# Kernel tuning notes

Hardware: AMD Instinct MI355X
Metric: run time of the kernel (lower is better)

## Reference

```python
import jax, jax.numpy as jnp
import numpy as np

B, TE, TD = 16, 400, 64
E, H = 256, 512
H2 = 2 * H  # 1024
V = 32000


def setup_inputs():
    key = jax.random.key(0)
    k = jax.random.split(key, 16)
    s = 0.05
    return {
        "encoder_inputs": jax.random.randint(k[0], (B, TE), 0, V),
        "decoder_inputs": jax.random.randint(k[1], (B, TD), 0, V),
        "ext_oov_sizes": jax.random.randint(k[2], (B,), 0, 10),
        "enc_idxes_on_ext_voc": jax.random.randint(k[3], (B, TE), 0, V),
        "h0": jnp.zeros((2, B, H), jnp.float32),
        "c0": jnp.zeros((2, B, H), jnp.float32),
        "emb": jax.random.normal(k[4], (V, E)) * 0.1,
        "Wih_f": jax.random.normal(k[5], (4 * H, E)) * s,
        "Whh_f": jax.random.normal(k[6], (4 * H, H)) * s,
        "b_f": jnp.zeros((4 * H,), jnp.float32),
        "Wih_b": jax.random.normal(k[7], (4 * H, E)) * s,
        "Whh_b": jax.random.normal(k[8], (4 * H, H)) * s,
        "b_b": jnp.zeros((4 * H,), jnp.float32),
        "Wih_d": jax.random.normal(k[9], (4 * H2, E + 2 * H2)) * s,
        "Whh_d": jax.random.normal(k[10], (4 * H2, H2)) * s,
        "b_d": jnp.zeros((4 * H2,), jnp.float32),
        "W_ea": jax.random.normal(k[11], (H2, H2)) * 0.006,
        "W_da": jax.random.normal(k[12], (H2, H2)) * 0.006,
        "W_v": jax.random.normal(k[13], (V, 3 * H2)) * s,
        "b_v": jnp.zeros((V,), jnp.float32),
    }


def lstm_cell(x, h, c, Wih, Whh, b):
    z = x @ Wih.T + h @ Whh.T + b
    i, f, g, o = jnp.split(z, 4, axis=-1)
    i, f, o = jax.nn.sigmoid(i), jax.nn.sigmoid(f), jax.nn.sigmoid(o)
    c2 = f * c + i * jnp.tanh(g)
    return o * jnp.tanh(c2), c2


def run_lstm(xs, h0, c0, Wih, Whh, b):
    # xs: [T, B, E]
    def step(carry, x):
        h, c = lstm_cell(x, carry[0], carry[1], Wih, Whh, b)
        return (h, c), h
    (h, c), hs = jax.lax.scan(step, (h0, c0), xs)
    return hs, h, c


def _forward(emb, Wih_f, Whh_f, b_f, Wih_b, Whh_b, b_b, Wih_d, Whh_d, b_d,
             W_ea, W_da, W_v, b_v, h0, c0, encoder_inputs, decoder_inputs):
    xs = emb[encoder_inputs].transpose(1, 0, 2)  # [TE, B, E]
    hs_f, hf, cf = run_lstm(xs, h0[0], c0[0], Wih_f, Whh_f, b_f)
    hs_b, hb, cb = run_lstm(xs[::-1], h0[1], c0[1], Wih_b, Whh_b, b_b)
    enc_out = jnp.concatenate([hs_f, hs_b[::-1]], axis=-1).transpose(1, 0, 2)  # [B, TE, 2H]
    h = jnp.concatenate([hf, hb], axis=-1)  # [B, 2H] (torch reshape of bi-dir last hidden)
    c = jnp.concatenate([cf, cb], axis=-1)
    dec_emb = emb[decoder_inputs].transpose(1, 0, 2)  # [TD, B, E]

    def step(carry, xs_t):
        h, c, accum, buf = carry
        i, emb_t = xs_t
        # intra-temporal encoder attention: exp scores normalized by past accumulation
        scores = jnp.einsum('bd,btd->bt', h @ W_ea, enc_out)  # [B, TE]
        exp_s = jnp.exp(scores)
        denom = jnp.where(i == 0, jnp.ones_like(accum), accum)
        ep = exp_s / denom
        attn = ep / jnp.sum(ep, axis=-1, keepdims=True)
        ctx_e = jnp.einsum('bt,btd->bd', attn, enc_out)
        # intra-decoder attention over previously produced hidden states (masked)
        dsc = jnp.einsum('bd,tbd->bt', h @ W_da, buf)  # [B, TD]
        dsc = jnp.where((jnp.arange(TD) < i)[None, :], dsc, -1e30)
        dw = jnp.where(i == 0, 0.0, jax.nn.softmax(dsc, axis=-1))
        ctx_d = jnp.einsum('bt,tbd->bd', dw, buf)
        x = jnp.concatenate([emb_t, ctx_e, ctx_d], axis=-1)  # [B, E+4H]
        h2, c2 = lstm_cell(x, h, c, Wih_d, Whh_d, b_d)
        buf2 = buf.at[i].set(h2)
        feat = jnp.concatenate([h2, ctx_e, ctx_d], axis=-1)  # [B, 6H]
        logd = jax.nn.log_softmax(feat @ W_v.T + b_v, axis=-1)
        return (h2, c2, accum + exp_s, buf2), logd

    carry0 = (h, c, jnp.zeros((B, TE), h.dtype), jnp.zeros((TD, B, H2), h.dtype))
    (h, c, _, _), logds = jax.lax.scan(step, carry0, (jnp.arange(TD), dec_emb))
    return logds.transpose(1, 0, 2), h[None], c[None]


def reference(encoder_inputs, decoder_inputs, ext_oov_sizes, enc_idxes_on_ext_voc,
              h0, c0, emb, Wih_f, Whh_f, b_f, Wih_b, Whh_b, b_b,
              Wih_d, Whh_d, b_d, W_ea, W_da, W_v, b_v):
    # ext_oov_sizes / enc_idxes_on_ext_voc are unused by forward (as in the torch source)
    return _forward(emb, Wih_f, Whh_f, b_f, Wih_b, Whh_b, b_b, Wih_d, Whh_d, b_d,
                    W_ea, W_da, W_v, b_v, h0, c0, encoder_inputs, decoder_inputs)
```

## Files before the change

### kernel.cpp

```cpp
#include <hip/hip_runtime.h>
#include <math.h>

#define B_  16
#define TE_ 400
#define TD_ 64
#define E_  256
#define H_  512
#define H2_ 1024
#define V_  32000

typedef __attribute__((ext_vector_type(4))) float f32x4;
typedef __attribute__((ext_vector_type(8))) short s16x8;
typedef __attribute__((ext_vector_type(8))) unsigned short u16x8;
typedef __attribute__((ext_vector_type(4))) unsigned short u16x4;

__device__ __forceinline__ float bf2f(unsigned short u){
  union { unsigned int i; float f; } v; v.i = ((unsigned int)u) << 16; return v.f;
}
__device__ __forceinline__ unsigned short f2bf(float f){
  union { float f; unsigned int i; } v; v.f = f;
  return (unsigned short)((v.i + 0x7fffu + ((v.i >> 16) & 1u)) >> 16);
}
__device__ __forceinline__ float sigmoidf_(float x){ return 1.f/(1.f + expf(-x)); }

__device__ __forceinline__ void gl_lds16(const void* gsrc, void* ldst){
  __builtin_amdgcn_global_load_lds(
      (const __attribute__((address_space(1))) unsigned int*)gsrc,
      (__attribute__((address_space(3))) unsigned int*)ldst, 16, 0, 0);
}

__device__ __forceinline__ void arrive8(unsigned* inst){
  __threadfence();
  __hip_atomic_fetch_add(inst + (blockIdx.x & 7u)*16, 1u, __ATOMIC_RELAXED, __HIP_MEMORY_SCOPE_AGENT);
}
__device__ __forceinline__ void poll8(unsigned* inst, unsigned target){
  int it = 0;
  for(;;){
    unsigned s = 0;
    #pragma unroll
    for (int k = 0; k < 8; ++k)
      s += __hip_atomic_load(inst + k*16, __ATOMIC_RELAXED, __HIP_MEMORY_SCOPE_AGENT);
    if (s >= target) break;
    if (it < 6) __builtin_amdgcn_s_sleep(1);
    else if (it < 24) __builtin_amdgcn_s_sleep(4);
    else __builtin_amdgcn_s_sleep(16);
    ++it;
  }
}

__global__ void k_init(unsigned* bars, float* ctxn, float* psumT){
  int gid = blockIdx.x*256 + threadIdx.x;
  if (gid < 81920) bars[gid] = 0u;
  if (gid < 32768) ctxn[gid] = 0.f;
  if (gid < 32) psumT[gid] = 0.f;
}

__global__ void k_gather(const float* __restrict__ emb, const int* __restrict__ idx,
                         unsigned short* __restrict__ out, int T){
  int wv = threadIdx.x >> 6, l = threadIdx.x & 63;
  int row = blockIdx.x*4 + wv;
  if (row >= T*B_) return;
  int t = row >> 4, b = row & 15;
  int tok = idx[b*T + t];
  float4 v = *(const float4*)(emb + (size_t)tok*E_ + l*4);
  u16x4 o; o[0]=f2bf(v.x); o[1]=f2bf(v.y); o[2]=f2bf(v.z); o[3]=f2bf(v.w);
  *(u16x4*)(out + (size_t)row*E_ + l*4) = o;
}

__global__ void k_prep_enc(const float* __restrict__ Wih_f, const float* __restrict__ Whh_f,
                           const float* __restrict__ Wih_b, const float* __restrict__ Whh_b,
                           unsigned short* __restrict__ Wenc){
  int it = blockIdx.x*256 + threadIdx.x;
  int dir = it / (2048*96); int rem = it % (2048*96);
  int pr = rem / 96; int kc = rem % 96; int k0 = kc*8;
  int g = pr >> 6, r = pr & 63, gate = r >> 4, ul = r & 15;
  int orig = gate*H_ + g*16 + ul;
  const float* Wih = dir ? Wih_b : Wih_f;
  const float* Whh = dir ? Whh_b : Whh_f;
  u16x8 o;
  #pragma unroll
  for (int e = 0; e < 8; ++e){
    int k = k0 + e;
    float v = (k < E_) ? Wih[(size_t)orig*E_ + k] : Whh[(size_t)orig*H_ + (k - E_)];
    o[e] = f2bf(v);
  }
  *(u16x8*)(Wenc + ((size_t)dir*2048 + pr)*768 + k0) = o;
}

__device__ __forceinline__ void prep_whext_item(int it, const float* __restrict__ Whh_d,
                                                const float* __restrict__ W_da,
                                                char* __restrict__ WhExt){
  if (it < 524288){
    int g = it >> 13; int rem = it & 8191;
    int kblk = rem >> 10; int rem2 = rem & 1023;
    int row = rem2 >> 4; int k8 = rem2 & 15;
    int gate = row >> 4, ul = row & 15;
    int orig = gate*H2_ + g*16 + ul;
    u16x8 o;
    #pragma unroll
    for (int e = 0; e < 8; ++e)
      o[e] = f2bf(Whh_d[(size_t)orig*H2_ + kblk*128 + k8*8 + e]);
    size_t off = (size_t)g*163840 + (size_t)kblk*20480 + (size_t)(row*256 + ((k8*16) ^ ((row&7)<<4)));
    *(u16x8*)(WhExt + off) = o;
  } else if (it < 655360){
    int qi = it - 524288;
    int g = qi >> 11; int rem = qi & 2047;
    int kblk = rem >> 8; int c2 = rem & 255;
    int wvv = c2 >> 6, rr = (c2 >> 2) & 15, c = c2 & 3;
    int row = g*16 + rr;
    u16x8 o;
    #pragma unroll
    for (int e = 0; e < 8; ++e)
      o[e] = f2bf(W_da[(size_t)row*H2_ + kblk*128 + wvv*32 + c*8 + e]);
    size_t off = (size_t)g*163840 + (size_t)kblk*20480 + 16384
               + (size_t)(wvv*1024 + rr*64 + ((c*16) ^ ((rr&3)<<4)));
    *(u16x8*)(WhExt + off) = o;
  }
}

__device__ __forceinline__ void prep_ctx_item(int it, const float* __restrict__ Wih_d,
                                              char* __restrict__ CtxW){
  int g = it >> 14; int rem = it & 16383;
  int kblk = rem >> 10; int rem2 = rem & 1023;
  int row = rem2 >> 4; int k8 = rem2 & 15;
  int gate = row >> 4, ul = row & 15;
  int orig = gate*H2_ + g*16 + ul;
  int k = 256 + kblk*128 + k8*8;
  u16x8 o;
  #pragma unroll
  for (int e = 0; e < 8; ++e)
    o[e] = f2bf(Wih_d[(size_t)orig*2304 + k + e]);
  size_t off = (size_t)g*262144 + (size_t)kblk*16384 + (size_t)(row*256 + ((k8*16) ^ ((row&7)<<4)));
  *(u16x8*)(CtxW + off) = o;
}

__global__ void k_prep_wihemb(const float* __restrict__ Wih_d, unsigned short* __restrict__ Wemb){
  int it = blockIdx.x*256 + threadIdx.x;
  int p = it >> 5; int k0 = (it & 31)*8;
  int g = p >> 6, gate = (p >> 4) & 3, ul = p & 15;
  int orig = gate*H2_ + g*16 + ul;
  u16x8 o;
  #pragma unroll
  for (int e = 0; e < 8; ++e)
    o[e] = f2bf(Wih_d[(size_t)orig*2304 + k0 + e]);
  *(u16x8*)(Wemb + (size_t)p*256 + k0) = o;
}

__global__ void __launch_bounds__(256, 2) k_zinit(
    const unsigned short* __restrict__ A,
    const unsigned short* __restrict__ Bw,
    const float* __restrict__ bd,
    float* __restrict__ Cz)
{
  __shared__ unsigned short Ab[128*72];
  __shared__ unsigned short Bt[128*72];
  int p = blockIdx.x;
  int mt = p >> 5, nt = p & 31;
  int m0 = mt*128, n0 = nt*128;
  int tid = threadIdx.x, wvv = tid>>6, l = tid&63;
  int wr = wvv>>1, wc = wvv&1;
  f32x4 zero4 = {0.f,0.f,0.f,0.f};
  f32x4 acc[4][4];
  #pragma unroll
  for (int a=0;a<4;++a){
    #pragma unroll
    for (int b=0;b<4;++b) acc[a][b] = zero4;
  }
  for (int k0 = 0; k0 < 256; k0 += 64){
    #pragma unroll
    for (int qq = 0; qq < 4; ++qq){
      int idx8 = (tid + qq*256)*8;
      int r = idx8 >> 6, k = idx8 & 63;
      *(u16x8*)(Ab + r*72 + k) = *(const u16x8*)(A + (size_t)(m0+r)*256 + k0 + k);
      *(u16x8*)(Bt + r*72 + k) = *(const u16x8*)(Bw + (size_t)(n0+r)*256 + k0 + k);
    }
    __syncthreads();
    #pragma unroll
    for (int ks = 0; ks < 2; ++ks){
      s16x8 af[4], bf[4];
      #pragma unroll
      for (int fi=0;fi<4;++fi)
        af[fi] = *(const s16x8*)(Ab + (wr*64+fi*16+(l&15))*72 + ks*32 + (l>>4)*8);
      #pragma unroll
      for (int fj=0;fj<4;++fj)
        bf[fj] = *(const s16x8*)(Bt + (wc*64+fj*16+(l&15))*72 + ks*32 + (l>>4)*8);
      #pragma unroll
      for (int fi=0;fi<4;++fi){
        #pragma unroll
        for (int fj=0;fj<4;++fj)
          acc[fi][fj] = __builtin_amdgcn_mfma_f32_16x16x32_bf16(af[fi], bf[fj], acc[fi][fj], 0,0,0);
      }
    }
    __syncthreads();
  }
  #pragma unroll
  for (int fj=0;fj<4;++fj){
    int col = n0 + wc*64 + fj*16 + (l&15);
    int orig = ((col>>4)&3)*H2_ + (col>>6)*16 + (col&15);
    float bias = bd[orig];
    #pragma unroll
    for (int fi=0;fi<4;++fi){
      #pragma unroll
      for (int j=0;j<4;++j){
        int row = m0 + wr*64 + fi*16 + (l>>4)*4 + j;
        Cz[(size_t)row*4096 + col] = acc[fi][fj][j] + bias;
      }
    }
  }
}

__global__ void __launch_bounds__(256, 2) k_zx(
    const unsigned short* __restrict__ xs,
    const unsigned short* __restrict__ Wenc,
    const float* __restrict__ b_f, const float* __restrict__ b_b,
    unsigned short* __restrict__ zx)
{
  __shared__ unsigned short Ab[128*72];
  __shared__ unsigned short Bt[128*72];
  int pblk = blockIdx.x;
  int dir = pblk / 800; int rem = pblk % 800;
  int mt = rem >> 4, nt = rem & 15;
  int m0 = mt*128, n0 = nt*128;
  int tid = threadIdx.x, wvv = tid>>6, l = tid&63;
  int wr = wvv>>1, wc = wvv&1;
  f32x4 zero4 = {0.f,0.f,0.f,0.f};
  f32x4 acc[4][4];
  #pragma unroll
  for (int a=0;a<4;++a){
    #pragma unroll
    for (int b=0;b<4;++b) acc[a][b] = zero4;
  }
  for (int k0 = 0; k0 < 256; k0 += 64){
    #pragma unroll
    for (int qq = 0; qq < 4; ++qq){
      int idx8 = (tid + qq*256)*8;
      int r = idx8 >> 6, k = idx8 & 63;
      *(u16x8*)(Ab + r*72 + k) = *(const u16x8*)(xs + (size_t)(m0+r)*256 + k0 + k);
      *(u16x8*)(Bt + r*72 + k) = *(const u16x8*)(Wenc + ((size_t)dir*2048 + n0+r)*768 + k0 + k);
    }
    __syncthreads();
    #pragma unroll
    for (int ks = 0; ks < 2; ++ks){
      s16x8 af[4], bf[4];
      #pragma unroll
      for (int fi=0;fi<4;++fi)
        af[fi] = *(const s16x8*)(Ab + (wr*64+fi*16+(l&15))*72 + ks*32 + (l>>4)*8);
      #pragma unroll
      for (int fj=0;fj<4;++fj)
        bf[fj] = *(const s16x8*)(Bt + (wc*64+fj*16+(l&15))*72 + ks*32 + (l>>4)*8);
      #pragma unroll
      for (int fi=0;fi<4;++fi){
        #pragma unroll
        for (int fj=0;fj<4;++fj)
          acc[fi][fj] = __builtin_amdgcn_mfma_f32_16x16x32_bf16(af[fi], bf[fj], acc[fi][fj], 0,0,0);
      }
    }
    __syncthreads();
  }
  const float* bsrc = dir ? b_b : b_f;
  #pragma unroll
  for (int fj=0;fj<4;++fj){
    int col = n0 + wc*64 + fj*16 + (l&15);
    float bias = bsrc[((col>>4)&3)*512 + (col>>6)*16 + (col&15)];
    #pragma unroll
    for (int fi=0;fi<4;++fi){
      #pragma unroll
      for (int j=0;j<4;++j){
        int row = m0 + wr*64 + fi*16 + (l>>4)*4 + j;
        zx[((size_t)dir*6400 + row)*2048 + col] = f2bf(acc[fi][fj][j] + bias);
      }
    }
  }
}

__global__ void __launch_bounds__(256, 2) k_penc(
    const unsigned short* __restrict__ enc,
    const float* __restrict__ Wea,
    unsigned short* __restrict__ P)
{
  __shared__ unsigned short Ab[128*72];
  __shared__ unsigned short Bt[128*72];
  int p = blockIdx.x;
  int mt = p >> 3, nt = p & 7;
  int m0 = mt*128, n0 = nt*128;
  int tid = threadIdx.x, wvv = tid>>6, l = tid&63;
  int wr = wvv>>1, wc = wvv&1;
  f32x4 zero4 = {0.f,0.f,0.f,0.f};
  f32x4 acc[4][4];
  #pragma unroll
  for (int a=0;a<4;++a){
    #pragma unroll
    for (int b=0;b<4;++b) acc[a][b] = zero4;
  }
  for (int k0 = 0; k0 < 1024; k0 += 64){
    #pragma unroll
    for (int qq = 0; qq < 4; ++qq){
      int idx8 = (tid + qq*256)*8;
      int r = idx8 >> 6, k = idx8 & 63;
      *(u16x8*)(Ab + r*72 + k) = *(const u16x8*)(enc + (size_t)(m0+r)*1024 + k0 + k);
    }
    #pragma unroll
    for (int qq = 0; qq < 4; ++qq){
      int idx8 = (tid + qq*256)*8;
      int r = idx8 >> 6, k = idx8 & 63;
      const float* src = Wea + (size_t)(n0+r)*1024 + k0 + k;
      float4 v0 = *(const float4*)src;
      float4 v1 = *(const float4*)(src+4);
      u16x8 o;
      o[0]=f2bf(v0.x); o[1]=f2bf(v0.y); o[2]=f2bf(v0.z); o[3]=f2bf(v0.w);
      o[4]=f2bf(v1.x); o[5]=f2bf(v1.y); o[6]=f2bf(v1.z); o[7]=f2bf(v1.w);
      *(u16x8*)(Bt + r*72 + k) = o;
    }
    __syncthreads();
    #pragma unroll
    for (int ks = 0; ks < 2; ++ks){
      s16x8 af[4], bf[4];
      #pragma unroll
      for (int fi=0;fi<4;++fi)
        af[fi] = *(const s16x8*)(Ab + (wr*64+fi*16+(l&15))*72 + ks*32 + (l>>4)*8);
      #pragma unroll
      for (int fj=0;fj<4;++fj)
        bf[fj] = *(const s16x8*)(Bt + (wc*64+fj*16+(l&15))*72 + ks*32 + (l>>4)*8);
      #pragma unroll
      for (int fi=0;fi<4;++fi){
        #pragma unroll
        for (int fj=0;fj<4;++fj)
          acc[fi][fj] = __builtin_amdgcn_mfma_f32_16x16x32_bf16(af[fi], bf[fj], acc[fi][fj], 0,0,0);
      }
    }
    __syncthreads();
  }
  #pragma unroll
  for (int fj=0;fj<4;++fj){
    int col = n0 + wc*64 + fj*16 + (l&15);
    #pragma unroll
    for (int fi=0;fi<4;++fi){
      #pragma unroll
      for (int j=0;j<4;++j){
        int row = m0 + wr*64 + fi*16 + (l>>4)*4 + j;
        P[(size_t)row*1024 + col] = f2bf(acc[fi][fj][j]);
      }
    }
  }
}

__global__ void __launch_bounds__(256, 1) k_encoder(
    const unsigned short* __restrict__ zx,
    const unsigned short* __restrict__ Wenc,
    const float* __restrict__ h0, const float* __restrict__ c0,
    unsigned short* __restrict__ enc_out,
    unsigned short* __restrict__ hbuf,
    float* __restrict__ h0dec, float* __restrict__ c0dec,
    unsigned* __restrict__ bars,
    const float* __restrict__ Whh_d, const float* __restrict__ W_da,
    const float* __restrict__ Wih_d,
    char* __restrict__ WhExt, char* __restrict__ CtxW)
{
  extern __shared__ char smem[];
  int tid = threadIdx.x;
  int w = blockIdx.x;
  if (w >= 64){
    int base = (w - 64)*256 + tid;
    for (int it = base; it < 655360; it += 36864) prep_whext_item(it, Whh_d, W_da, WhExt);
    for (int it = base; it < 1048576; it += 36864) prep_ctx_item(it, Wih_d, CtxW);
    return;
  }
  unsigned short* Wt = (unsigned short*)smem;
  unsigned short* At = Wt + 64*520;
  float* zl = (float*)(At + 16*520);
  int dir = w >> 5, g = w & 31;
  int wv = tid >> 6, l = tid & 63;
  {
    const unsigned short* Wsrc = Wenc + ((size_t)dir*2048 + g*64)*768 + 256;
    int r = tid >> 2, s = tid & 3;
    for (int c = 0; c < 16; ++c)
      *(u16x8*)(Wt + r*520 + s*128 + c*8) = *(const u16x8*)(Wsrc + (size_t)r*768 + s*128 + c*8);
  }
  int bb = tid >> 4, ul = tid & 15;
  float creg = c0[((size_t)dir*16 + bb)*H_ + g*16 + ul];
  int kchunk = (l >> 4) * 8;
  f32x4 zero4 = { 0.f, 0.f, 0.f, 0.f };
  {
    int r = tid >> 4, s = tid & 15;
    for (int e = 0; e < 32; ++e)
      At[r*520 + s*32 + e] = f2bf(h0[((size_t)dir*16 + r)*H_ + s*32 + e]);
  }
  int tg0 = dir ? (TE_-1) : 0;
  const unsigned short* zrow = zx + ((size_t)dir*6400 + (size_t)tg0*16 + (l>>4)*4)*2048 + g*64 + wv*16 + (l&15);
  f32x4 a0cur;
  a0cur[0]=bf2f(zrow[0]); a0cur[1]=bf2f(zrow[2048]); a0cur[2]=bf2f(zrow[4096]); a0cur[3]=bf2f(zrow[6144]);
  __syncthreads();
  for (int t = 0; t < TE_; ++t){
    int tg = dir ? (TE_-1 - t) : t;
    f32x4 acc0 = a0cur, acc1 = zero4;
    const unsigned short* brow = Wt + (wv*16 + (l&15))*520 + kchunk;
    const unsigned short* ap   = At + (l&15)*520 + kchunk;
    #pragma unroll
    for (int ks = 0; ks < 16; ++ks){
      s16x8 afr = *(const s16x8*)(ap + ks*32);
      s16x8 bfr = *(const s16x8*)(brow + ks*32);
      if (ks & 1) acc1 = __builtin_amdgcn_mfma_f32_16x16x32_bf16(afr, bfr, acc1, 0, 0, 0);
      else        acc0 = __builtin_amdgcn_mfma_f32_16x16x32_bf16(afr, bfr, acc0, 0, 0, 0);
    }
    f32x4 acc = acc0 + acc1;
    #pragma unroll
    for (int j = 0; j < 4; ++j)
      zl[wv*256 + ((l>>4)*4 + j)*16 + (l&15)] = acc[j];
    __syncthreads();
    float zi = zl[0*256 + bb*16 + ul];
    float zf = zl[1*256 + bb*16 + ul];
    float zg = zl[2*256 + bb*16 + ul];
    float zo = zl[3*256 + bb*16 + ul];
    float iv = sigmoidf_(zi), fv = sigmoidf_(zf), gv = tanhf(zg), ov = sigmoidf_(zo);
    float cc = fv*creg + iv*gv;
    float hh = ov * tanhf(cc);
    creg = cc;
    int u = g*16 + ul;
    unsigned short hb = f2bf(hh);
    hbuf[((size_t)dir*2 + ((t+1)&1))*(16*H_) + bb*H_ + u] = hb;
    enc_out[((size_t)bb*TE_ + tg)*H2_ + dir*H_ + u] = hb;
    if (t == TE_-1){
      h0dec[(size_t)bb*H2_ + dir*H_ + u] = hh;
      c0dec[(size_t)bb*H2_ + dir*H_ + u] = cc;
    }
    unsigned* cnt = bars + (size_t)(dir*400 + t)*64;
    __syncthreads();
    if (tid == 0){
      __threadfence();
      __hip_atomic_fetch_add(cnt + (g&3)*16, 1u, __ATOMIC_RELAXED, __HIP_MEMORY_SCOPE_AGENT);
    }
    if (t+1 < TE_){
      int tg2 = dir ? (TE_-2 - t) : (t+1);
      const unsigned short* zr2 = zx + ((size_t)dir*6400 + (size_t)tg2*16 + (l>>4)*4)*2048 + g*64 + wv*16 + (l&15);
      a0cur[0]=bf2f(zr2[0]); a0cur[1]=bf2f(zr2[2048]); a0cur[2]=bf2f(zr2[4096]); a0cur[3]=bf2f(zr2[6144]);
    }
    if (tid == 0){
      int it = 0;
      for(;;){
        unsigned s_ = 0;
        #pragma unroll
        for (int k2 = 0; k2 < 4; ++k2)
          s_ += __hip_atomic_load(cnt + k2*16, __ATOMIC_RELAXED, __HIP_MEMORY_SCOPE_AGENT);
        if (s_ >= 32) break;
        if (it < 6) __builtin_amdgcn_s_sleep(1);
        else __builtin_amdgcn_s_sleep(4);
        ++it;
      }
      __threadfence();
    }
    __syncthreads();
    if (t+1 < TE_){
      int r = tid >> 4, s = tid & 15;
      const unsigned short* hsrc = hbuf + ((size_t)dir*2 + ((t+1)&1))*(16*H_) + r*H_ + s*32;
      for (int c = 0; c < 4; ++c)
        *(u16x8*)(At + r*520 + s*32 + c*8) = *(const u16x8*)(hsrc + c*8);
    }
    __syncthreads();
  }
}

__global__ void k_dec_init(const float* __restrict__ h0dec, unsigned short* __restrict__ hreg){
  int gid = blockIdx.x*256 + threadIdx.x;
  if (gid < 16384) hreg[gid] = f2bf(h0dec[gid]);
}

__device__ __forceinline__ void issueA(const char* gA, char* BbA, int wv, int l, int kblk, int buf){
  const char* gsrc = gA + (size_t)kblk*20480;
  char* lb = BbA + buf*20480;
  #pragma unroll
  for (int q = 0; q < 4; ++q)
    gl_lds16(gsrc + wv*4096 + q*1024 + (size_t)l*16, lb + wv*4096 + q*1024);
  gl_lds16(gsrc + 16384 + wv*1024 + (size_t)l*16, lb + 16384 + wv*1024);
}
__device__ __forceinline__ void issueC(const char* gC, char* BbC, int wv, int l, int kblk, int buf){
  const char* gsrc = gC + (size_t)kblk*16384;
  char* lb = BbC + buf*16384;
  #pragma unroll
  for (int q = 0; q < 4; ++q)
    gl_lds16(gsrc + wv*4096 + q*1024 + (size_t)l*16, lb + wv*4096 + q*1024);
}

__global__ void __launch_bounds__(256, 1) k_decoder(
  const char* __restrict__ WhExt,
  const char* __restrict__ CtxW,
  const float* __restrict__ zinit,
  const unsigned short* __restrict__ Penc,
  const unsigned short* __restrict__ enc_out,
  const float* __restrict__ c0dec,
  unsigned short* __restrict__ hreg,
  unsigned short* __restrict__ xbuf,
  float* __restrict__ ctxn,
  float* __restrict__ psumT,
  unsigned short* __restrict__ vbuf,
  unsigned short* __restrict__ bufh,
  unsigned short* __restrict__ Av,
  float* __restrict__ outHC,
  unsigned* __restrict__ bars)
{
  extern __shared__ char smem[];
  int tid = threadIdx.x, w = blockIdx.x;
  int wv = tid >> 6, l = tid & 63;
  unsigned* dbase = bars + 51200;

  unsigned short* Atc = (unsigned short*)smem;
  unsigned short* Ah  = (unsigned short*)smem;
  char* BbA = smem + 66560;
  char* BbC = smem + 128000;
  float* zq = (float*)(smem + 66560);
  float* zl = (float*)(smem + 128000);
  unsigned short* encL = (unsigned short*)smem;
  float* epL  = (float*)(smem + 103424);
  float* accL = (float*)(smem + 103680);
  float* dscL = (float*)smem;

  bool isZ = (w < 64);
  bool isE = (w >= 64 && w < 192);
  int eb = 0, ec = 0;
  if (isE){ eb = (w-64) >> 3; ec = (w-64) & 7; }
  int db = w - 192;

  if (isE){
    for (int rr = 0; rr < 50; ++rr){
      const unsigned short* src = enc_out + ((size_t)eb*TE_ + ec*50 + rr)*H2_;
      *(u16x4*)(encL + rr*1032 + tid*4) = *(const u16x4*)(src + tid*4);
    }
    if (tid < 50) accL[tid] = 0.f;
    __syncthreads();
  }
  float creg = 0.f;
  int bb = tid >> 4, ul = tid & 15;
  const char* gA = WhExt + (size_t)w*163840;
  const char* gC = CtxW + (size_t)w*262144;
  f32x4 acc0, acc1;

  for (int i = 0; i < TD_; ++i){
    int p = i & 1;
    unsigned* barM = dbase + (size_t)(i*3+0)*128;
    unsigned* barA = dbase + (size_t)(i*3+1)*128;
    unsigned* barB = dbase + (size_t)(i*3+2)*128;

    if (isZ){
      ctxn[(p^1)*16384 + w*256 + tid] = 0.f;
      if (w == 0 && tid < 16) psumT[(p^1)*16 + tid] = 0.f;
      const float* zsrc = zinit + ((size_t)i*16 + (l>>4)*4)*4096 + w*64 + wv*16 + (l&15);
      f32x4 a0i; a0i[0]=zsrc[0]; a0i[1]=zsrc[4096]; a0i[2]=zsrc[8192]; a0i[3]=zsrc[12288];
      issueA(gA, BbA, wv, l, 0, 0);
      issueA(gA, BbA, wv, l, 1, 1);
      {
        int r = tid >> 4, s = tid & 15;
        const unsigned short* hsrc = hreg + p*16384 + r*H2_ + s*64;
        for (int c = 0; c < 8; ++c)
          *(u16x8*)(Ah + r*1032 + s*64 + c*8) = *(const u16x8*)(hsrc + c*8);
      }
      __syncthreads();
      acc0 = a0i;
      f32x4 z4 = {0.f,0.f,0.f,0.f};
      acc1 = z4;
      f32x4 accv = z4;
      int swz = ((l&7)<<4);
      for (int kblk = 0; kblk < 8; ++kblk){
        int buf = kblk % 3;
        if (kblk + 2 < 8) issueA(gA, BbA, wv, l, kblk+2, (kblk+2)%3);
        if (kblk < 6)       asm volatile("s_waitcnt vmcnt(10)" ::: "memory");
        else if (kblk == 6) asm volatile("s_waitcnt vmcnt(5)" ::: "memory");
        else                asm volatile("s_waitcnt vmcnt(0)" ::: "memory");
        const unsigned short* ap = Ah + (l&15)*1032 + kblk*128 + (l>>4)*8;
        const char* Bz = BbA + buf*20480 + wv*4096;
        #pragma unroll
        for (int ks = 0; ks < 4; ++ks){
          int k8 = ks*4 + (l>>4);
          s16x8 afr = *(const s16x8*)(ap + ks*32);
          s16x8 bfr = *(const s16x8*)(Bz + (l&15)*256 + ((k8*16) ^ swz));
          if (ks & 1) acc1 = __builtin_amdgcn_mfma_f32_16x16x32_bf16(afr, bfr, acc1, 0,0,0);
          else        acc0 = __builtin_amdgcn_mfma_f32_16x16x32_bf16(afr, bfr, acc0, 0,0,0);
        }
        s16x8 afq = *(const s16x8*)(Ah + (l&15)*1032 + kblk*128 + wv*32 + (l>>4)*8);
        s16x8 bfv = *(const s16x8*)(BbA + buf*20480 + 16384 + wv*1024 + (l&15)*64 + ((((l>>4)*16)) ^ ((l&3)<<4)));
        accv = __builtin_amdgcn_mfma_f32_16x16x32_bf16(afq, bfv, accv, 0,0,0);
      }
      __syncthreads();
      #pragma unroll
      for (int j = 0; j < 4; ++j)
        zq[wv*256 + ((l>>4)*4+j)*16 + (l&15)] = accv[j];
      __syncthreads();
      if (i > 0){
        float vv = zq[0*256+bb*16+ul] + zq[1*256+bb*16+ul] + zq[2*256+bb*16+ul] + zq[3*256+bb*16+ul];
        vbuf[((size_t)(i-1)*16 + bb)*H2_ + w*16 + ul] = f2bf(vv);
      }
      __syncthreads();
      if (tid == 0) arrive8(barM);
      issueC(gC, BbC, wv, l, 0, 0);
      issueC(gC, BbC, wv, l, 1, 1);
      if (tid == 0){ poll8(barA, 144); __threadfence(); }
      __syncthreads();
      {
        int r = tid >> 4, s = tid & 15;
        float inv = 1.f / psumT[p*16 + r];
        const float* cn = ctxn + p*16384 + (size_t)r*1024 + s*64;
        for (int c8 = 0; c8 < 8; ++c8){
          float4 v0 = *(const float4*)(cn + c8*8);
          float4 v1 = *(const float4*)(cn + c8*8 + 4);
          u16x8 o;
          o[0]=f2bf(v0.x*inv); o[1]=f2bf(v0.y*inv); o[2]=f2bf(v0.z*inv); o[3]=f2bf(v0.w*inv);
          o[4]=f2bf(v1.x*inv); o[5]=f2bf(v1.y*inv); o[6]=f2bf(v1.z*inv); o[7]=f2bf(v1.w*inv);
          *(u16x8*)(Atc + r*2056 + s*64 + c8*8) = o;
        }
        const unsigned short* xd = xbuf + (size_t)r*1024 + s*64;
        for (int c8 = 0; c8 < 8; ++c8)
          *(u16x8*)(Atc + r*2056 + 1024 + s*64 + c8*8) = *(const u16x8*)(xd + c8*8);
      }
      {
        float val = ctxn[p*16384 + (size_t)bb*1024 + w*16 + ul] / psumT[p*16 + bb];
        Av[((size_t)bb*TD_ + i)*3072 + 1024 + w*16 + ul] = f2bf(val);
      }
      __syncthreads();
      for (int k = 0; k < 16; ++k){
        if (k < 15) asm volatile("s_waitcnt vmcnt(4)" ::: "memory");
        else        asm volatile("s_waitcnt vmcnt(0)" ::: "memory");
        const unsigned short* ap = Atc + (l&15)*2056 + k*128 + (l>>4)*8;
        const char* Bz = BbC + (k&1)*16384 + wv*4096;
        #pragma unroll
        for (int ks = 0; ks < 4; ++ks){
          int k8 = ks*4 + (l>>4);
          s16x8 afr = *(const s16x8*)(ap + ks*32);
          s16x8 bfr = *(const s16x8*)(Bz + (l&15)*256 + ((k8*16) ^ swz));
          if (ks & 1) acc1 = __builtin_amdgcn_mfma_f32_16x16x32_bf16(afr, bfr, acc1, 0,0,0);
          else        acc0 = __builtin_amdgcn_mfma_f32_16x16x32_bf16(afr, bfr, acc0, 0,0,0);
        }
        if (k + 2 < 16) issueC(gC, BbC, wv, l, k+2, k&1);
      }
      __syncthreads();
      f32x4 acc = acc0 + acc1;
      #pragma unroll
      for (int j = 0; j < 4; ++j)
        zl[wv*256 + ((l>>4)*4+j)*16 + (l&15)] = acc[j];
      __syncthreads();
      float zi = zl[0*256 + bb*16 + ul];
      float zf = zl[1*256 + bb*16 + ul];
      float zg = zl[2*256 + bb*16 + ul];
      float zo = zl[3*256 + bb*16 + ul];
      if (i == 0) creg = c0dec[(size_t)bb*H2_ + w*16 + ul];
      float iv = sigmoidf_(zi), fv = sigmoidf_(zf), gv = tanhf(zg), ov = sigmoidf_(zo);
      float cc = fv*creg + iv*gv;
      float hh = ov*tanhf(cc);
      creg = cc;
      int u = w*16 + ul;
      unsigned short hb2 = f2bf(hh);
      hreg[((i+1)&1)*16384 + (size_t)bb*H2_ + u] = hb2;
      Av[((size_t)bb*TD_ + i)*3072 + u] = hb2;
      bufh[((size_t)i*16 + bb)*H2_ + u] = hb2;
      if (i == TD_-1){
        outHC[(size_t)bb*H2_ + u] = hh;
        outHC[16384 + (size_t)bb*H2_ + u] = cc;
      }
      __syncthreads();
      if (tid == 0){ arrive8(barB); poll8(barB, 64); __threadfence(); }
      __syncthreads();
    } else if (isE){
      const unsigned short* hb_ = hreg + p*16384 + eb*H2_ + l*16;
      u16x8 hv0 = *(const u16x8*)hb_;
      u16x8 hv1 = *(const u16x8*)(hb_ + 8);
      float hf[16];
      #pragma unroll
      for (int c = 0; c < 8; ++c){ hf[c] = bf2f(hv0[c]); hf[8+c] = bf2f(hv1[c]); }
      for (int rr = wv; rr < 50; rr += 4){
        const unsigned short* pr = Penc + ((size_t)(eb*TE_ + ec*50 + rr))*H2_ + l*16;
        u16x8 p0 = *(const u16x8*)pr;
        u16x8 p1 = *(const u16x8*)(pr + 8);
        float sc = 0.f;
        #pragma unroll
        for (int c = 0; c < 8; ++c) sc += hf[c]*bf2f(p0[c]);
        #pragma unroll
        for (int c = 0; c < 8; ++c) sc += hf[8+c]*bf2f(p1[c]);
        #pragma unroll
        for (int o = 1; o < 64; o <<= 1) sc += __shfl_xor(sc, o);
        if (l == 0){
          float es = expf(sc);
          float aold = accL[rr];
          float denom = (i == 0) ? 1.f : aold;
          accL[rr] = aold + es;
          epL[rr] = es / denom;
        }
      }
      __syncthreads();
      float tot = 0.f;
      for (int rr = 0; rr < 50; ++rr) tot += epL[rr];
      float a0=0.f,a1=0.f,a2=0.f,a3=0.f;
      for (int rr = 0; rr < 50; ++rr){
        float wgt = epL[rr];
        u16x4 ev = *(const u16x4*)(encL + rr*1032 + tid*4);
        a0 += wgt*bf2f(ev[0]); a1 += wgt*bf2f(ev[1]); a2 += wgt*bf2f(ev[2]); a3 += wgt*bf2f(ev[3]);
      }
      float* dst = ctxn + p*16384 + (size_t)eb*1024 + tid*4;
      atomicAdd(dst+0, a0); atomicAdd(dst+1, a1); atomicAdd(dst+2, a2); atomicAdd(dst+3, a3);
      if (tid == 0) atomicAdd(psumT + p*16 + eb, tot);
      __syncthreads();
      if (tid == 0){ arrive8(barA); poll8(barB, 64); __threadfence(); }
      __syncthreads();
    } else {
      int col = tid*4;
      if (i == 0){
        u16x4 z4v = {0,0,0,0};
        *(u16x4*)(xbuf + (size_t)db*1024 + col) = z4v;
        *(u16x4*)(Av + ((size_t)db*TD_ + i)*3072 + 2048 + col) = z4v;
      } else {
        if (tid == 0){ poll8(barM, 64); __threadfence(); }
        __syncthreads();
        const unsigned short* hq = hreg + p*16384 + db*H2_ + l*16;
        u16x8 h0v = *(const u16x8*)hq;
        u16x8 h1v = *(const u16x8*)(hq + 8);
        float qf[16];
        #pragma unroll
        for (int c = 0; c < 8; ++c){ qf[c] = bf2f(h0v[c]); qf[8+c] = bf2f(h1v[c]); }
        for (int tp = wv; tp < i; tp += 4){
          const unsigned short* vr = vbuf + ((size_t)tp*16 + db)*H2_ + l*16;
          u16x8 e0 = *(const u16x8*)vr;
          u16x8 e1 = *(const u16x8*)(vr + 8);
          float sc = 0.f;
          #pragma unroll
          for (int c = 0; c < 8; ++c) sc += qf[c]*bf2f(e0[c]);
          #pragma unroll
          for (int c = 0; c < 8; ++c) sc += qf[8+c]*bf2f(e1[c]);
          #pragma unroll
          for (int o = 1; o < 64; o <<= 1) sc += __shfl_xor(sc, o);
          if (l == 0) dscL[tp] = sc;
        }
        __syncthreads();
        float scv = (l < i) ? dscL[l] : -1e30f;
        float m = scv;
        #pragma unroll
        for (int o = 1; o < 64; o <<= 1) m = fmaxf(m, __shfl_xor(m, o));
        float e = (l < i) ? expf(scv - m) : 0.f;
        float ssum = e;
        #pragma unroll
        for (int o = 1; o < 64; o <<= 1) ssum += __shfl_xor(ssum, o);
        float wgt = e / ssum;
        float c0_=0.f,c1_=0.f,c2_=0.f,c3_=0.f;
        for (int tp = 0; tp < i; ++tp){
          float wt = __shfl(wgt, tp);
          u16x4 hv = *(const u16x4*)(bufh + ((size_t)tp*16 + db)*H2_ + col);
          c0_ += wt*bf2f(hv[0]); c1_ += wt*bf2f(hv[1]); c2_ += wt*bf2f(hv[2]); c3_ += wt*bf2f(hv[3]);
        }
        u16x4 o4; o4[0]=f2bf(c0_); o4[1]=f2bf(c1_); o4[2]=f2bf(c2_); o4[3]=f2bf(c3_);
        *(u16x4*)(xbuf + (size_t)db*1024 + col) = o4;
        *(u16x4*)(Av + ((size_t)db*TD_ + i)*3072 + 2048 + col) = o4;
      }
      __syncthreads();
      if (tid == 0){ arrive8(barA); poll8(barB, 64); __threadfence(); }
      __syncthreads();
    }
  }
}

__global__ void __launch_bounds__(256, 2) k_vocab_gemm(
    const unsigned short* __restrict__ Av,
    const float* __restrict__ Wv,
    const float* __restrict__ bv,
    float* __restrict__ out)
{
  __shared__ unsigned short Ab[128*72];
  __shared__ unsigned short Bt[128*72];
  int p = blockIdx.x;
  int mt = (p>>3)&7, nt = (p&7) + 8*(p>>6);
  if (nt >= 250) return;
  int m0 = mt*128, n0 = nt*128;
  int tid = threadIdx.x, wvv = tid>>6, l = tid&63;
  int wr = wvv>>1, wc = wvv&1;
  f32x4 zero4 = {0.f,0.f,0.f,0.f};
  f32x4 acc[4][4];
  #pragma unroll
  for (int a=0;a<4;++a){
    #pragma unroll
    for (int b=0;b<4;++b) acc[a][b] = zero4;
  }
  for (int k0 = 0; k0 < 3072; k0 += 64){
    #pragma unroll
    for (int qq = 0; qq < 4; ++qq){
      int idx8 = (tid + qq*256)*8;
      int r = idx8 >> 6, k = idx8 & 63;
      *(u16x8*)(Ab + r*72 + k) = *(const u16x8*)(Av + (size_t)(m0+r)*3072 + k0 + k);
    }
    #pragma unroll
    for (int qq = 0; qq < 4; ++qq){
      int idx8 = (tid + qq*256)*8;
      int r = idx8 >> 6, k = idx8 & 63;
      const float* src = Wv + (size_t)(n0+r)*3072 + k0 + k;
      float4 v0 = *(const float4*)src;
      float4 v1 = *(const float4*)(src+4);
      u16x8 o;
      o[0]=f2bf(v0.x); o[1]=f2bf(v0.y); o[2]=f2bf(v0.z); o[3]=f2bf(v0.w);
      o[4]=f2bf(v1.x); o[5]=f2bf(v1.y); o[6]=f2bf(v1.z); o[7]=f2bf(v1.w);
      *(u16x8*)(Bt + r*72 + k) = o;
    }
    __syncthreads();
    #pragma unroll
    for (int ks = 0; ks < 2; ++ks){
      s16x8 af[4], bf[4];
      #pragma unroll
      for (int fi=0;fi<4;++fi)
        af[fi] = *(const s16x8*)(Ab + (wr*64+fi*16+(l&15))*72 + ks*32 + (l>>4)*8);
      #pragma unroll
      for (int fj=0;fj<4;++fj)
        bf[fj] = *(const s16x8*)(Bt + (wc*64+fj*16+(l&15))*72 + ks*32 + (l>>4)*8);
      #pragma unroll
      for (int fi=0;fi<4;++fi){
        #pragma unroll
        for (int fj=0;fj<4;++fj)
          acc[fi][fj] = __builtin_amdgcn_mfma_f32_16x16x32_bf16(af[fi], bf[fj], acc[fi][fj], 0,0,0);
      }
    }
    __syncthreads();
  }
  #pragma unroll
  for (int fj=0;fj<4;++fj){
    int col = n0 + wc*64 + fj*16 + (l&15);
    float bias = bv[col];
    #pragma unroll
    for (int fi=0;fi<4;++fi){
      #pragma unroll
      for (int j=0;j<4;++j){
        int row = m0 + wr*64 + fi*16 + (l>>4)*4 + j;
        out[(size_t)row*V_ + col] = acc[fi][fj][j] + bias;
      }
    }
  }
}

__global__ void k_logsoftmax(float* __restrict__ out){
  int row = blockIdx.x;
  float* x = out + (size_t)row*V_;
  int tid = threadIdx.x;
  __shared__ float red[64];
  float m = -1e30f;
  for (int c = tid; c < V_; c += 256) m = fmaxf(m, x[c]);
  #pragma unroll
  for (int o=1;o<64;o<<=1) m = fmaxf(m, __shfl_xor(m,o));
  if ((tid&63)==0) red[tid>>6] = m;
  __syncthreads();
  m = fmaxf(fmaxf(red[0],red[1]), fmaxf(red[2],red[3]));
  float s = 0.f;
  for (int c = tid; c < V_; c += 256) s += expf(x[c]-m);
  #pragma unroll
  for (int o=1;o<64;o<<=1) s += __shfl_xor(s,o);
  if ((tid&63)==0) red[8 + (tid>>6)] = s;
  __syncthreads();
  s = red[8]+red[9]+red[10]+red[11];
  float lse = m + logf(s);
  for (int c = tid; c < V_; c += 256) x[c] = x[c] - lse;
}

extern "C" void kernel_launch(void* const* d_in, const int* in_sizes, int n_in,
                              void* d_out, int out_size, void* d_ws, size_t ws_size,
                              hipStream_t stream){
  (void)in_sizes; (void)n_in; (void)out_size; (void)ws_size;
  const int*   enc_in = (const int*)d_in[0];
  const int*   dec_in = (const int*)d_in[1];
  const float* h0   = (const float*)d_in[4];
  const float* c0   = (const float*)d_in[5];
  const float* emb  = (const float*)d_in[6];
  const float* Wih_f= (const float*)d_in[7];
  const float* Whh_f= (const float*)d_in[8];
  const float* b_f  = (const float*)d_in[9];
  const float* Wih_b= (const float*)d_in[10];
  const float* Whh_b= (const float*)d_in[11];
  const float* b_b  = (const float*)d_in[12];
  const float* Wih_d= (const float*)d_in[13];
  const float* Whh_d= (const float*)d_in[14];
  const float* b_d  = (const float*)d_in[15];
  const float* W_ea = (const float*)d_in[16];
  const float* W_da = (const float*)d_in[17];
  const float* W_v  = (const float*)d_in[18];
  const float* b_v  = (const float*)d_in[19];
  float* out = (float*)d_out;
  char* ws = (char*)d_ws;

  size_t o_bars   = 0;
  size_t o_ctxn   = 327680;
  size_t o_psumT  = o_ctxn + 131072;
  size_t o_xs     = o_psumT + 256;
  size_t o_decemb = o_xs + (size_t)6400*256*2;
  size_t o_Wenc   = o_decemb + (size_t)1024*256*2;
  size_t o_WhExt  = o_Wenc + (size_t)2*2048*768*2;
  size_t o_CtxW   = o_WhExt + (size_t)64*163840;
  size_t o_Wemb   = o_CtxW + (size_t)64*262144;
  size_t o_zinit  = o_Wemb + (size_t)4096*256*2;
  size_t o_zx     = o_zinit + (size_t)1024*4096*4;
  size_t o_enc    = o_zx + (size_t)2*6400*2048*2;
  size_t o_Penc   = o_enc + (size_t)16*400*1024*2;
  size_t o_hbuf   = o_Penc + (size_t)16*400*1024*2;
  size_t o_h0dec  = o_hbuf + (size_t)2*2*16*512*2;
  size_t o_c0dec  = o_h0dec + (size_t)16*1024*4;
  size_t o_hreg   = o_c0dec + (size_t)16*1024*4;
  size_t o_xbuf   = o_hreg + (size_t)2*16*1024*2;
  size_t o_vbuf   = o_xbuf + (size_t)16*1024*2;
  size_t o_bufh   = o_vbuf + (size_t)64*16*1024*2;
  size_t o_Av     = o_bufh + (size_t)64*16*1024*2;

  unsigned* bars        = (unsigned*)(ws + o_bars);
  float* ctxn           = (float*)(ws + o_ctxn);
  float* psumT          = (float*)(ws + o_psumT);
  unsigned short* xs    = (unsigned short*)(ws + o_xs);
  unsigned short* decemb= (unsigned short*)(ws + o_decemb);
  unsigned short* Wenc  = (unsigned short*)(ws + o_Wenc);
  char* WhExt           = ws + o_WhExt;
  char* CtxW            = ws + o_CtxW;
  unsigned short* Wemb  = (unsigned short*)(ws + o_Wemb);
  float* zinit          = (float*)(ws + o_zinit);
  unsigned short* zx    = (unsigned short*)(ws + o_zx);
  unsigned short* encO  = (unsigned short*)(ws + o_enc);
  unsigned short* Penc  = (unsigned short*)(ws + o_Penc);
  unsigned short* hbuf  = (unsigned short*)(ws + o_hbuf);
  float* h0dec          = (float*)(ws + o_h0dec);
  float* c0dec          = (float*)(ws + o_c0dec);
  unsigned short* hreg  = (unsigned short*)(ws + o_hreg);
  unsigned short* xbuf  = (unsigned short*)(ws + o_xbuf);
  unsigned short* vbuf  = (unsigned short*)(ws + o_vbuf);
  unsigned short* bufh  = (unsigned short*)(ws + o_bufh);
  unsigned short* Av    = (unsigned short*)(ws + o_Av);

  hipFuncSetAttribute((const void*)k_encoder, hipFuncAttributeMaxDynamicSharedMemorySize, 90000);
  hipFuncSetAttribute((const void*)k_decoder, hipFuncAttributeMaxDynamicSharedMemorySize, 160768);

  k_init<<<320, 256, 0, stream>>>(bars, ctxn, psumT);
  k_gather<<<1600, 256, 0, stream>>>(emb, enc_in, xs, TE_);
  k_gather<<<256, 256, 0, stream>>>(emb, dec_in, decemb, TD_);
  k_prep_enc<<<1536, 256, 0, stream>>>(Wih_f, Whh_f, Wih_b, Whh_b, Wenc);
  k_prep_wihemb<<<512, 256, 0, stream>>>(Wih_d, Wemb);
  k_zinit<<<256, 256, 0, stream>>>(decemb, Wemb, b_d, zinit);
  k_zx<<<1600, 256, 0, stream>>>(xs, Wenc, b_f, b_b, zx);
  k_encoder<<<208, 256, 87296, stream>>>(zx, Wenc, h0, c0, encO, hbuf, h0dec, c0dec, bars,
                                         Whh_d, W_da, Wih_d, WhExt, CtxW);
  k_penc<<<400, 256, 0, stream>>>(encO, W_ea, Penc);
  k_dec_init<<<64, 256, 0, stream>>>(h0dec, hreg);
  k_decoder<<<208, 256, 160768, stream>>>(WhExt, CtxW, zinit, Penc, encO, c0dec,
                                          hreg, xbuf, ctxn, psumT, vbuf, bufh, Av,
                                          out + (size_t)32768000, bars);
  k_vocab_gemm<<<2048, 256, 0, stream>>>(Av, W_v, b_v, out);
  k_logsoftmax<<<1024, 256, 0, stream>>>(out);
}
```

Measured before the change: 5.538 ms.

## Split decoder gate GEMM across two block groups with partial-sum exchange

The decoder's per-step LSTM gate matmul is divided between two groups of 64 blocks: group A handles the attention projection plus the first half of Whh and the first half of the context weights, and group B handles the rest. The halves are combined through a global partial-sum buffer. Weights are repacked into per-wave contiguous slabs and streamed with a 4-deep LDS pipeline. Barrier counters are spread out to cut atomic contention, and the grid grows from 208 to 256 blocks with less shared memory per block. This halves the weight bytes each gate block streams per step, at the cost of an extra cross-block reduction and synchronisation.

```diff
diff --git a/kernel.cpp b/kernel.cpp
--- a/kernel.cpp
+++ b/kernel.cpp
@@ -28,29 +28,35 @@
       (const __attribute__((address_space(1))) unsigned int*)gsrc,
       (__attribute__((address_space(3))) unsigned int*)ldst, 16, 0, 0);
 }
-
-__device__ __forceinline__ void arrive8(unsigned* inst){
+__device__ __forceinline__ void issue4(const char* gsrc, char* ldst, int l){
+  #pragma unroll
+  for (int q = 0; q < 4; ++q)
+    gl_lds16(gsrc + q*1024 + (size_t)l*16, ldst + q*1024);
+}
+
+__device__ __forceinline__ void d_arrive(unsigned* bars, int inst){
   __threadfence();
-  __hip_atomic_fetch_add(inst + (blockIdx.x & 7u)*16, 1u, __ATOMIC_RELAXED, __HIP_MEMORY_SCOPE_AGENT);
-}
-__device__ __forceinline__ void poll8(unsigned* inst, unsigned target){
+  __hip_atomic_fetch_add(bars + (blockIdx.x & 7u)*4096 + inst*16, 1u, __ATOMIC_RELAXED, __HIP_MEMORY_SCOPE_AGENT);
+}
+__device__ __forceinline__ void d_poll(unsigned* bars, int inst, unsigned tgt){
   int it = 0;
   for(;;){
     unsigned s = 0;
     #pragma unroll
     for (int k = 0; k < 8; ++k)
-      s += __hip_atomic_load(inst + k*16, __ATOMIC_RELAXED, __HIP_MEMORY_SCOPE_AGENT);
-    if (s >= target) break;
+      s += __hip_atomic_load(bars + k*4096 + inst*16, __ATOMIC_RELAXED, __HIP_MEMORY_SCOPE_AGENT);
+    if (s >= tgt) break;
     if (it < 6) __builtin_amdgcn_s_sleep(1);
     else if (it < 24) __builtin_amdgcn_s_sleep(4);
     else __builtin_amdgcn_s_sleep(16);
     ++it;
   }
+  __threadfence();
 }
 
 __global__ void k_init(unsigned* bars, float* ctxn, float* psumT){
   int gid = blockIdx.x*256 + threadIdx.x;
-  if (gid < 81920) bars[gid] = 0u;
+  if (gid < 99328) bars[gid] = 0u;
   if (gid < 32768) ctxn[gid] = 0.f;
   if (gid < 32) psumT[gid] = 0.f;
 }
@@ -87,51 +93,58 @@
   *(u16x8*)(Wenc + ((size_t)dir*2048 + pr)*768 + k0) = o;
 }
 
-__device__ __forceinline__ void prep_whext_item(int it, const float* __restrict__ Whh_d,
-                                                const float* __restrict__ W_da,
-                                                char* __restrict__ WhExt){
-  if (it < 524288){
-    int g = it >> 13; int rem = it & 8191;
-    int kblk = rem >> 10; int rem2 = rem & 1023;
-    int row = rem2 >> 4; int k8 = rem2 & 15;
-    int gate = row >> 4, ul = row & 15;
-    int orig = gate*H2_ + g*16 + ul;
-    u16x8 o;
-    #pragma unroll
-    for (int e = 0; e < 8; ++e)
-      o[e] = f2bf(Whh_d[(size_t)orig*H2_ + kblk*128 + k8*8 + e]);
-    size_t off = (size_t)g*163840 + (size_t)kblk*20480 + (size_t)(row*256 + ((k8*16) ^ ((row&7)<<4)));
-    *(u16x8*)(WhExt + off) = o;
-  } else if (it < 655360){
-    int qi = it - 524288;
-    int g = qi >> 11; int rem = qi & 2047;
-    int kblk = rem >> 8; int c2 = rem & 255;
-    int wvv = c2 >> 6, rr = (c2 >> 2) & 15, c = c2 & 3;
-    int row = g*16 + rr;
-    u16x8 o;
-    #pragma unroll
-    for (int e = 0; e < 8; ++e)
-      o[e] = f2bf(W_da[(size_t)row*H2_ + kblk*128 + wvv*32 + c*8 + e]);
-    size_t off = (size_t)g*163840 + (size_t)kblk*20480 + 16384
-               + (size_t)(wvv*1024 + rr*64 + ((c*16) ^ ((rr&3)<<4)));
-    *(u16x8*)(WhExt + off) = o;
-  }
-}
-
-__device__ __forceinline__ void prep_ctx_item(int it, const float* __restrict__ Wih_d,
-                                              char* __restrict__ CtxW){
-  int g = it >> 14; int rem = it & 16383;
-  int kblk = rem >> 10; int rem2 = rem & 1023;
-  int row = rem2 >> 4; int k8 = rem2 & 15;
-  int gate = row >> 4, ul = row & 15;
-  int orig = gate*H2_ + g*16 + ul;
-  int k = 256 + kblk*128 + k8*8;
+__device__ __forceinline__ void prep_SA_item(int it, const float* __restrict__ Whh_d,
+                                             const float* __restrict__ W_da, char* __restrict__ SA){
+  int g = it / 6144; int r = it % 6144;
+  int wv = r / 1536; int r2 = r % 1536;
+  int sb = r2 >> 8; int e = r2 & 255;
+  int row = e >> 4, k8 = e & 15;
   u16x8 o;
-  #pragma unroll
-  for (int e = 0; e < 8; ++e)
-    o[e] = f2bf(Wih_d[(size_t)orig*2304 + k + e]);
-  size_t off = (size_t)g*262144 + (size_t)kblk*16384 + (size_t)(row*256 + ((k8*16) ^ ((row&7)<<4)));
-  *(u16x8*)(CtxW + off) = o;
+  if (sb < 2){
+    int k = wv*256 + sb*128 + k8*8;
+    #pragma unroll
+    for (int e2 = 0; e2 < 8; ++e2)
+      o[e2] = f2bf(W_da[(size_t)(g*16 + row)*H2_ + k + e2]);
+  } else {
+    int orig = wv*H2_ + g*16 + row;
+    int k = (sb-2)*128 + k8*8;
+    #pragma unroll
+    for (int e2 = 0; e2 < 8; ++e2)
+      o[e2] = f2bf(Whh_d[(size_t)orig*H2_ + k + e2]);
+  }
+  size_t off = (size_t)g*98304 + (size_t)wv*24576 + (size_t)sb*4096
+             + (size_t)(row*256 + ((k8*16) ^ ((row&7)<<4)));
+  *(u16x8*)(SA + off) = o;
+}
+__device__ __forceinline__ void prep_SB_item(int it, const float* __restrict__ Whh_d,
+                                             char* __restrict__ SB){
+  int g = it >> 12; int r = it & 4095;
+  int wv = r >> 10; int sb = (r >> 8) & 3; int e = r & 255;
+  int row = e >> 4, k8 = e & 15;
+  int orig = wv*H2_ + g*16 + row;
+  int k = 512 + sb*128 + k8*8;
+  u16x8 o;
+  #pragma unroll
+  for (int e2 = 0; e2 < 8; ++e2)
+    o[e2] = f2bf(Whh_d[(size_t)orig*H2_ + k + e2]);
+  size_t off = (size_t)g*65536 + (size_t)wv*16384 + (size_t)sb*4096
+             + (size_t)(row*256 + ((k8*16) ^ ((row&7)<<4)));
+  *(u16x8*)(SB + off) = o;
+}
+__device__ __forceinline__ void prep_C_item(int it, const float* __restrict__ Wih_d,
+                                            char* __restrict__ C, int colbase){
+  int g = it >> 13; int r = it & 8191;
+  int wv = r >> 11; int sb = (r >> 8) & 7; int e = r & 255;
+  int row = e >> 4, k8 = e & 15;
+  int orig = wv*H2_ + g*16 + row;
+  int col = colbase + sb*128 + k8*8;
+  u16x8 o;
+  #pragma unroll
+  for (int e2 = 0; e2 < 8; ++e2)
+    o[e2] = f2bf(Wih_d[(size_t)orig*2304 + col + e2]);
+  size_t off = (size_t)g*131072 + (size_t)wv*32768 + (size_t)sb*4096
+             + (size_t)(row*256 + ((k8*16) ^ ((row&7)<<4)));
+  *(u16x8*)(C + off) = o;
 }
 
 __global__ void k_prep_wihemb(const float* __restrict__ Wih_d, unsigned short* __restrict__ Wemb){
@@ -354,15 +367,18 @@
     unsigned* __restrict__ bars,
     const float* __restrict__ Whh_d, const float* __restrict__ W_da,
     const float* __restrict__ Wih_d,
-    char* __restrict__ WhExt, char* __restrict__ CtxW)
+    char* __restrict__ SA, char* __restrict__ SB,
+    char* __restrict__ CA, char* __restrict__ CB)
 {
   extern __shared__ char smem[];
   int tid = threadIdx.x;
   int w = blockIdx.x;
   if (w >= 64){
     int base = (w - 64)*256 + tid;
-    for (int it = base; it < 655360; it += 36864) prep_whext_item(it, Whh_d, W_da, WhExt);
-    for (int it = base; it < 1048576; it += 36864) prep_ctx_item(it, Wih_d, CtxW);
+    for (int it = base; it < 393216; it += 36864) prep_SA_item(it, Whh_d, W_da, SA);
+    for (int it = base; it < 262144; it += 36864) prep_SB_item(it, Whh_d, SB);
+    for (int it = base; it < 524288; it += 36864) prep_C_item(it, Wih_d, CA, 256);
+    for (int it = base; it < 524288; it += 36864) prep_C_item(it, Wih_d, CB, 1280);
     return;
   }
   unsigned short* Wt = (unsigned short*)smem;
@@ -370,6 +386,7 @@
   float* zl = (float*)(At + 16*520);
   int dir = w >> 5, g = w & 31;
   int wv = tid >> 6, l = tid & 63;
+  unsigned* ebars = bars + 32768;
   {
     const unsigned short* Wsrc = Wenc + ((size_t)dir*2048 + g*64)*768 + 256;
     int r = tid >> 2, s = tid & 3;
@@ -423,11 +440,11 @@
       h0dec[(size_t)bb*H2_ + dir*H_ + u] = hh;
       c0dec[(size_t)bb*H2_ + dir*H_ + u] = cc;
     }
-    unsigned* cnt = bars + (size_t)(dir*400 + t)*64;
+    int inst = dir*400 + t;
     __syncthreads();
     if (tid == 0){
       __threadfence();
-      __hip_atomic_fetch_add(cnt + (g&3)*16, 1u, __ATOMIC_RELAXED, __HIP_MEMORY_SCOPE_AGENT);
+      __hip_atomic_fetch_add(ebars + (g&3)*16384 + inst*16, 1u, __ATOMIC_RELAXED, __HIP_MEMORY_SCOPE_AGENT);
     }
     if (t+1 < TE_){
       int tg2 = dir ? (TE_-2 - t) : (t+1);
@@ -440,7 +457,7 @@
         unsigned s_ = 0;
         #pragma unroll
         for (int k2 = 0; k2 < 4; ++k2)
-          s_ += __hip_atomic_load(cnt + k2*16, __ATOMIC_RELAXED, __HIP_MEMORY_SCOPE_AGENT);
+          s_ += __hip_atomic_load(ebars + k2*16384 + inst*16, __ATOMIC_RELAXED, __HIP_MEMORY_SCOPE_AGENT);
         if (s_ >= 32) break;
         if (it < 6) __builtin_amdgcn_s_sleep(1);
         else __builtin_amdgcn_s_sleep(4);
@@ -464,25 +481,9 @@
   if (gid < 16384) hreg[gid] = f2bf(h0dec[gid]);
 }
 
-__device__ __forceinline__ void issueA(const char* gA, char* BbA, int wv, int l, int kblk, int buf){
-  const char* gsrc = gA + (size_t)kblk*20480;
-  char* lb = BbA + buf*20480;
-  #pragma unroll
-  for (int q = 0; q < 4; ++q)
-    gl_lds16(gsrc + wv*4096 + q*1024 + (size_t)l*16, lb + wv*4096 + q*1024);
-  gl_lds16(gsrc + 16384 + wv*1024 + (size_t)l*16, lb + 16384 + wv*1024);
-}
-__device__ __forceinline__ void issueC(const char* gC, char* BbC, int wv, int l, int kblk, int buf){
-  const char* gsrc = gC + (size_t)kblk*16384;
-  char* lb = BbC + buf*16384;
-  #pragma unroll
-  for (int q = 0; q < 4; ++q)
-    gl_lds16(gsrc + wv*4096 + q*1024 + (size_t)l*16, lb + wv*4096 + q*1024);
-}
-
 __global__ void __launch_bounds__(256, 1) k_decoder(
-  const char* __restrict__ WhExt,
-  const char* __restrict__ CtxW,
+  const char* __restrict__ SA, const char* __restrict__ SB,
+  const char* __restrict__ CA, const char* __restrict__ CB,
   const float* __restrict__ zinit,
   const unsigned short* __restrict__ Penc,
   const unsigned short* __restrict__ enc_out,
@@ -495,168 +496,198 @@
   unsigned short* __restrict__ bufh,
   unsigned short* __restrict__ Av,
   float* __restrict__ outHC,
+  float* __restrict__ pz,
   unsigned* __restrict__ bars)
 {
   extern __shared__ char smem[];
   int tid = threadIdx.x, w = blockIdx.x;
   int wv = tid >> 6, l = tid & 63;
-  unsigned* dbase = bars + 51200;
-
-  unsigned short* Atc = (unsigned short*)smem;
-  unsigned short* Ah  = (unsigned short*)smem;
-  char* BbA = smem + 66560;
-  char* BbC = smem + 128000;
-  float* zq = (float*)(smem + 66560);
-  float* zl = (float*)(smem + 128000);
-  unsigned short* encL = (unsigned short*)smem;
-  float* epL  = (float*)(smem + 103424);
-  float* accL = (float*)(smem + 103680);
-  float* dscL = (float*)smem;
-
-  bool isZ = (w < 64);
-  bool isE = (w >= 64 && w < 192);
-  int eb = 0, ec = 0;
-  if (isE){ eb = (w-64) >> 3; ec = (w-64) & 7; }
-  int db = w - 192;
-
-  if (isE){
-    for (int rr = 0; rr < 50; ++rr){
-      const unsigned short* src = enc_out + ((size_t)eb*TE_ + ec*50 + rr)*H2_;
-      *(u16x4*)(encL + rr*1032 + tid*4) = *(const u16x4*)(src + tid*4);
-    }
-    if (tid < 50) accL[tid] = 0.f;
-    __syncthreads();
-  }
-  float creg = 0.f;
   int bb = tid >> 4, ul = tid & 15;
-  const char* gA = WhExt + (size_t)w*163840;
-  const char* gC = CtxW + (size_t)w*262144;
-  f32x4 acc0, acc1;
-
-  for (int i = 0; i < TD_; ++i){
-    int p = i & 1;
-    unsigned* barM = dbase + (size_t)(i*3+0)*128;
-    unsigned* barA = dbase + (size_t)(i*3+1)*128;
-    unsigned* barB = dbase + (size_t)(i*3+2)*128;
-
-    if (isZ){
-      ctxn[(p^1)*16384 + w*256 + tid] = 0.f;
-      if (w == 0 && tid < 16) psumT[(p^1)*16 + tid] = 0.f;
-      const float* zsrc = zinit + ((size_t)i*16 + (l>>4)*4)*4096 + w*64 + wv*16 + (l&15);
-      f32x4 a0i; a0i[0]=zsrc[0]; a0i[1]=zsrc[4096]; a0i[2]=zsrc[8192]; a0i[3]=zsrc[12288];
-      issueA(gA, BbA, wv, l, 0, 0);
-      issueA(gA, BbA, wv, l, 1, 1);
-      {
-        int r = tid >> 4, s = tid & 15;
-        const unsigned short* hsrc = hreg + p*16384 + r*H2_ + s*64;
+  unsigned* flags = bars + 98304;
+
+  if (w < 128){
+    bool isA = (w < 64);
+    int g = isA ? w : (w - 64);
+    unsigned short* Ah = (unsigned short*)smem;
+    char* myB = smem + 33024 + wv*16384;
+    float* zlv = (float*)(smem + 98560);
+    float* zlg = (float*)(smem + 102656);
+    const char* myS1 = isA ? (SA + (size_t)g*98304 + (size_t)wv*24576)
+                           : (SB + (size_t)g*65536 + (size_t)wv*16384);
+    const char* myC  = isA ? (CA + (size_t)g*131072 + (size_t)wv*32768)
+                           : (CB + (size_t)g*131072 + (size_t)wv*32768);
+    int nsub1 = isA ? 6 : 4;
+    int swz = ((l&7)<<4);
+    float creg = 0.f;
+
+    for (int i = 0; i < TD_; ++i){
+      int p = i & 1;
+      int iM = i*3, iAb = i*3+1, iBb = i*3+2;
+      f32x4 z4 = {0.f,0.f,0.f,0.f};
+      f32x4 accg = z4, accv = z4;
+      if (isA){
+        ctxn[(p^1)*16384 + g*256 + tid] = 0.f;
+        if (g == 0 && tid < 16) psumT[(p^1)*16 + tid] = 0.f;
+        const float* zsrc = zinit + ((size_t)i*16 + (l>>4)*4)*4096 + g*64 + wv*16 + (l&15);
+        accg[0]=zsrc[0]; accg[1]=zsrc[4096]; accg[2]=zsrc[8192]; accg[3]=zsrc[12288];
+      }
+      #pragma unroll
+      for (int sb = 0; sb < 4; ++sb)
+        issue4(myS1 + sb*4096, myB + sb*4096, l);
+      { int r = tid >> 4, s2 = tid & 15;
+        const unsigned short* hsrc = hreg + p*16384 + r*H2_ + s2*64;
         for (int c = 0; c < 8; ++c)
-          *(u16x8*)(Ah + r*1032 + s*64 + c*8) = *(const u16x8*)(hsrc + c*8);
+          *(u16x8*)(Ah + r*1032 + s2*64 + c*8) = *(const u16x8*)(hsrc + c*8);
       }
       __syncthreads();
-      acc0 = a0i;
-      f32x4 z4 = {0.f,0.f,0.f,0.f};
-      acc1 = z4;
-      f32x4 accv = z4;
-      int swz = ((l&7)<<4);
-      for (int kblk = 0; kblk < 8; ++kblk){
-        int buf = kblk % 3;
-        if (kblk + 2 < 8) issueA(gA, BbA, wv, l, kblk+2, (kblk+2)%3);
-        if (kblk < 6)       asm volatile("s_waitcnt vmcnt(10)" ::: "memory");
-        else if (kblk == 6) asm volatile("s_waitcnt vmcnt(5)" ::: "memory");
-        else                asm volatile("s_waitcnt vmcnt(0)" ::: "memory");
-        const unsigned short* ap = Ah + (l&15)*1032 + kblk*128 + (l>>4)*8;
-        const char* Bz = BbA + buf*20480 + wv*4096;
+      for (int s = 0; s < nsub1; ++s){
+        int rem = nsub1 - 1 - s;
+        if (rem >= 3)      asm volatile("s_waitcnt vmcnt(12)" ::: "memory");
+        else if (rem == 2) asm volatile("s_waitcnt vmcnt(8)" ::: "memory");
+        else if (rem == 1) asm volatile("s_waitcnt vmcnt(4)" ::: "memory");
+        else               asm volatile("s_waitcnt vmcnt(0)" ::: "memory");
+        int Koff = isA ? ((s < 2) ? (wv*256 + s*128) : ((s-2)*128)) : (512 + s*128);
+        const unsigned short* ap = Ah + (l&15)*1032 + Koff + (l>>4)*8;
+        const char* Bz = myB + (s&3)*4096;
+        if (isA && s < 2){
+          #pragma unroll
+          for (int ks = 0; ks < 4; ++ks){
+            int k8 = ks*4 + (l>>4);
+            s16x8 afr = *(const s16x8*)(ap + ks*32);
+            s16x8 bfr = *(const s16x8*)(Bz + (l&15)*256 + ((k8*16) ^ swz));
+            accv = __builtin_amdgcn_mfma_f32_16x16x32_bf16(afr, bfr, accv, 0,0,0);
+          }
+        } else {
+          #pragma unroll
+          for (int ks = 0; ks < 4; ++ks){
+            int k8 = ks*4 + (l>>4);
+            s16x8 afr = *(const s16x8*)(ap + ks*32);
+            s16x8 bfr = *(const s16x8*)(Bz + (l&15)*256 + ((k8*16) ^ swz));
+            accg = __builtin_amdgcn_mfma_f32_16x16x32_bf16(afr, bfr, accg, 0,0,0);
+          }
+        }
+        __builtin_amdgcn_sched_barrier(0);
+        if (s + 4 < nsub1) issue4(myS1 + (s+4)*4096, myB + ((s+4)&3)*4096, l);
+      }
+      if (isA){
         #pragma unroll
-        for (int ks = 0; ks < 4; ++ks){
-          int k8 = ks*4 + (l>>4);
-          s16x8 afr = *(const s16x8*)(ap + ks*32);
-          s16x8 bfr = *(const s16x8*)(Bz + (l&15)*256 + ((k8*16) ^ swz));
-          if (ks & 1) acc1 = __builtin_amdgcn_mfma_f32_16x16x32_bf16(afr, bfr, acc1, 0,0,0);
-          else        acc0 = __builtin_amdgcn_mfma_f32_16x16x32_bf16(afr, bfr, acc0, 0,0,0);
+        for (int j = 0; j < 4; ++j)
+          zlv[wv*256 + ((l>>4)*4+j)*16 + (l&15)] = accv[j];
+        __syncthreads();
+        if (i > 0){
+          float vv = zlv[bb*16+ul] + zlv[256+bb*16+ul] + zlv[512+bb*16+ul] + zlv[768+bb*16+ul];
+          vbuf[((size_t)(i-1)*16 + bb)*H2_ + g*16 + ul] = f2bf(vv);
         }
-        s16x8 afq = *(const s16x8*)(Ah + (l&15)*1032 + kblk*128 + wv*32 + (l>>4)*8);
-        s16x8 bfv = *(const s16x8*)(BbA + buf*20480 + 16384 + wv*1024 + (l&15)*64 + ((((l>>4)*16)) ^ ((l&3)<<4)));
-        accv = __builtin_amdgcn_mfma_f32_16x16x32_bf16(afq, bfv, accv, 0,0,0);
-      }
+        __syncthreads();
+        if (tid == 0) d_arrive(bars, iM);
+      }
+      #pragma unroll
+      for (int sb = 0; sb < 4; ++sb)
+        issue4(myC + sb*4096, myB + sb*4096, l);
+      if (tid == 0) d_poll(bars, iAb, 128);
       __syncthreads();
-      #pragma unroll
-      for (int j = 0; j < 4; ++j)
-        zq[wv*256 + ((l>>4)*4+j)*16 + (l&15)] = accv[j];
-      __syncthreads();
-      if (i > 0){
-        float vv = zq[0*256+bb*16+ul] + zq[1*256+bb*16+ul] + zq[2*256+bb*16+ul] + zq[3*256+bb*16+ul];
-        vbuf[((size_t)(i-1)*16 + bb)*H2_ + w*16 + ul] = f2bf(vv);
-      }
-      __syncthreads();
-      if (tid == 0) arrive8(barM);
-      issueC(gC, BbC, wv, l, 0, 0);
-      issueC(gC, BbC, wv, l, 1, 1);
-      if (tid == 0){ poll8(barA, 144); __threadfence(); }
-      __syncthreads();
-      {
-        int r = tid >> 4, s = tid & 15;
+      if (isA){
+        int r = tid >> 4, s2 = tid & 15;
         float inv = 1.f / psumT[p*16 + r];
-        const float* cn = ctxn + p*16384 + (size_t)r*1024 + s*64;
+        const float* cn = ctxn + p*16384 + (size_t)r*1024 + s2*64;
         for (int c8 = 0; c8 < 8; ++c8){
           float4 v0 = *(const float4*)(cn + c8*8);
           float4 v1 = *(const float4*)(cn + c8*8 + 4);
           u16x8 o;
           o[0]=f2bf(v0.x*inv); o[1]=f2bf(v0.y*inv); o[2]=f2bf(v0.z*inv); o[3]=f2bf(v0.w*inv);
           o[4]=f2bf(v1.x*inv); o[5]=f2bf(v1.y*inv); o[6]=f2bf(v1.z*inv); o[7]=f2bf(v1.w*inv);
-          *(u16x8*)(Atc + r*2056 + s*64 + c8*8) = o;
+          *(u16x8*)(Ah + r*1032 + s2*64 + c8*8) = o;
         }
-        const unsigned short* xd = xbuf + (size_t)r*1024 + s*64;
+        float val = ctxn[p*16384 + (size_t)bb*1024 + g*16 + ul] / psumT[p*16 + bb];
+        Av[((size_t)bb*TD_ + i)*3072 + 1024 + g*16 + ul] = f2bf(val);
+      } else {
+        int r = tid >> 4, s2 = tid & 15;
+        const unsigned short* xd = xbuf + (size_t)r*1024 + s2*64;
         for (int c8 = 0; c8 < 8; ++c8)
-          *(u16x8*)(Atc + r*2056 + 1024 + s*64 + c8*8) = *(const u16x8*)(xd + c8*8);
-      }
-      {
-        float val = ctxn[p*16384 + (size_t)bb*1024 + w*16 + ul] / psumT[p*16 + bb];
-        Av[((size_t)bb*TD_ + i)*3072 + 1024 + w*16 + ul] = f2bf(val);
+          *(u16x8*)(Ah + r*1032 + s2*64 + c8*8) = *(const u16x8*)(xd + c8*8);
       }
       __syncthreads();
-      for (int k = 0; k < 16; ++k){
-        if (k < 15) asm volatile("s_waitcnt vmcnt(4)" ::: "memory");
-        else        asm volatile("s_waitcnt vmcnt(0)" ::: "memory");
-        const unsigned short* ap = Atc + (l&15)*2056 + k*128 + (l>>4)*8;
-        const char* Bz = BbC + (k&1)*16384 + wv*4096;
+      for (int s = 0; s < 8; ++s){
+        int rem = 7 - s;
+        if (rem >= 3)      asm volatile("s_waitcnt vmcnt(12)" ::: "memory");
+        else if (rem == 2) asm volatile("s_waitcnt vmcnt(8)" ::: "memory");
+        else if (rem == 1) asm volatile("s_waitcnt vmcnt(4)" ::: "memory");
+        else               asm volatile("s_waitcnt vmcnt(0)" ::: "memory");
+        const unsigned short* ap = Ah + (l&15)*1032 + s*128 + (l>>4)*8;
+        const char* Bz = myB + (s&3)*4096;
         #pragma unroll
         for (int ks = 0; ks < 4; ++ks){
           int k8 = ks*4 + (l>>4);
           s16x8 afr = *(const s16x8*)(ap + ks*32);
           s16x8 bfr = *(const s16x8*)(Bz + (l&15)*256 + ((k8*16) ^ swz));
-          if (ks & 1) acc1 = __builtin_amdgcn_mfma_f32_16x16x32_bf16(afr, bfr, acc1, 0,0,0);
-          else        acc0 = __builtin_amdgcn_mfma_f32_16x16x32_bf16(afr, bfr, acc0, 0,0,0);
+          accg = __builtin_amdgcn_mfma_f32_16x16x32_bf16(afr, bfr, accg, 0,0,0);
         }
-        if (k + 2 < 16) issueC(gC, BbC, wv, l, k+2, k&1);
-      }
+        __builtin_amdgcn_sched_barrier(0);
+        if (s + 4 < 8) issue4(myC + (s+4)*4096, myB + ((s+4)&3)*4096, l);
+      }
+      #pragma unroll
+      for (int j = 0; j < 4; ++j)
+        zlg[wv*256 + ((l>>4)*4+j)*16 + (l&15)] = accg[j];
       __syncthreads();
-      f32x4 acc = acc0 + acc1;
-      #pragma unroll
-      for (int j = 0; j < 4; ++j)
-        zl[wv*256 + ((l>>4)*4+j)*16 + (l&15)] = acc[j];
+      if (isA){
+        if (tid == 0){
+          int it = 0;
+          while (__hip_atomic_load(flags + g*16, __ATOMIC_ACQUIRE, __HIP_MEMORY_SCOPE_AGENT) < (unsigned)(i+1)){
+            if (it < 8) __builtin_amdgcn_s_sleep(1);
+            else __builtin_amdgcn_s_sleep(4);
+            ++it;
+          }
+          __threadfence();
+        }
+        __syncthreads();
+        const float* pzg = pz + (size_t)g*1024;
+        float zi = zlg[0*256 + bb*16 + ul] + pzg[0*256 + bb*16 + ul];
+        float zf = zlg[1*256 + bb*16 + ul] + pzg[1*256 + bb*16 + ul];
+        float zg_ = zlg[2*256 + bb*16 + ul] + pzg[2*256 + bb*16 + ul];
+        float zo = zlg[3*256 + bb*16 + ul] + pzg[3*256 + bb*16 + ul];
+        if (i == 0) creg = c0dec[(size_t)bb*H2_ + g*16 + ul];
+        float iv = sigmoidf_(zi), fv = sigmoidf_(zf), gv = tanhf(zg_), ov = sigmoidf_(zo);
+        float cc = fv*creg + iv*gv;
+        float hh = ov*tanhf(cc);
+        creg = cc;
+        int u = g*16 + ul;
+        unsigned short hb2 = f2bf(hh);
+        hreg[((i+1)&1)*16384 + (size_t)bb*H2_ + u] = hb2;
+        Av[((size_t)bb*TD_ + i)*3072 + u] = hb2;
+        bufh[((size_t)i*16 + bb)*H2_ + u] = hb2;
+        if (i == TD_-1){
+          outHC[(size_t)bb*H2_ + u] = hh;
+          outHC[16384 + (size_t)bb*H2_ + u] = cc;
+        }
+        __syncthreads();
+        if (tid == 0) d_arrive(bars, iBb);
+      } else {
+        *(float4*)(pz + (size_t)g*1024 + tid*4) = *(const float4*)(zlg + tid*4);
+        __syncthreads();
+        if (tid == 0){
+          __threadfence();
+          __hip_atomic_store(flags + g*16, (unsigned)(i+1), __ATOMIC_RELEASE, __HIP_MEMORY_SCOPE_AGENT);
+        }
+      }
+      if (tid == 0) d_poll(bars, iBb, 64);
       __syncthreads();
-      float zi = zl[0*256 + bb*16 + ul];
-      float zf = zl[1*256 + bb*16 + ul];
-      float zg = zl[2*256 + bb*16 + ul];
-      float zo = zl[3*256 + bb*16 + ul];
-      if (i == 0) creg = c0dec[(size_t)bb*H2_ + w*16 + ul];
-      float iv = sigmoidf_(zi), fv = sigmoidf_(zf), gv = tanhf(zg), ov = sigmoidf_(zo);
-      float cc = fv*creg + iv*gv;
-      float hh = ov*tanhf(cc);
-      creg = cc;
-      int u = w*16 + ul;
-      unsigned short hb2 = f2bf(hh);
-      hreg[((i+1)&1)*16384 + (size_t)bb*H2_ + u] = hb2;
-      Av[((size_t)bb*TD_ + i)*3072 + u] = hb2;
-      bufh[((size_t)i*16 + bb)*H2_ + u] = hb2;
-      if (i == TD_-1){
-        outHC[(size_t)bb*H2_ + u] = hh;
-        outHC[16384 + (size_t)bb*H2_ + u] = cc;
-      }
-      __syncthreads();
-      if (tid == 0){ arrive8(barB); poll8(barB, 64); __threadfence(); }
-      __syncthreads();
-    } else if (isE){
+    }
+  } else {
+    int eb = (w-128) >> 3, ec = (w-128) & 7;
+    bool isDec = (ec == 0);
+    unsigned short* encL = (unsigned short*)smem;
+    float* epL  = (float*)(smem + 103232);
+    float* accL = (float*)(smem + 103488);
+    float* dscL = (float*)(smem + 103744);
+    for (int rr = 0; rr < 50; ++rr){
+      const unsigned short* src = enc_out + ((size_t)eb*TE_ + ec*50 + rr)*H2_;
+      *(u16x4*)(encL + rr*1032 + tid*4) = *(const u16x4*)(src + tid*4);
+    }
+    if (tid < 50) accL[tid] = 0.f;
+    __syncthreads();
+    for (int i = 0; i < TD_; ++i){
+      int p = i & 1;
+      int iM = i*3, iAb = i*3+1, iBb = i*3+2;
       const unsigned short* hb_ = hreg + p*16384 + eb*H2_ + l*16;
       u16x8 hv0 = *(const u16x8*)hb_;
       u16x8 hv1 = *(const u16x8*)(hb_ + 8);
@@ -695,58 +726,59 @@
       atomicAdd(dst+0, a0); atomicAdd(dst+1, a1); atomicAdd(dst+2, a2); atomicAdd(dst+3, a3);
       if (tid == 0) atomicAdd(psumT + p*16 + eb, tot);
       __syncthreads();
-      if (tid == 0){ arrive8(barA); poll8(barB, 64); __threadfence(); }
-      __syncthreads();
-    } else {
-      int col = tid*4;
-      if (i == 0){
-        u16x4 z4v = {0,0,0,0};
-        *(u16x4*)(xbuf + (size_t)db*1024 + col) = z4v;
-        *(u16x4*)(Av + ((size_t)db*TD_ + i)*3072 + 2048 + col) = z4v;
-      } else {
-        if (tid == 0){ poll8(barM, 64); __threadfence(); }
-        __syncthreads();
-        const unsigned short* hq = hreg + p*16384 + db*H2_ + l*16;
-        u16x8 h0v = *(const u16x8*)hq;
-        u16x8 h1v = *(const u16x8*)(hq + 8);
-        float qf[16];
-        #pragma unroll
-        for (int c = 0; c < 8; ++c){ qf[c] = bf2f(h0v[c]); qf[8+c] = bf2f(h1v[c]); }
-        for (int tp = wv; tp < i; tp += 4){
-          const unsigned short* vr = vbuf + ((size_t)tp*16 + db)*H2_ + l*16;
-          u16x8 e0 = *(const u16x8*)vr;
-          u16x8 e1 = *(const u16x8*)(vr + 8);
-          float sc = 0.f;
+      if (isDec){
+        int db = eb;
+        int col = tid*4;
+        if (i == 0){
+          u16x4 z4v = {0,0,0,0};
+          *(u16x4*)(xbuf + (size_t)db*1024 + col) = z4v;
+          *(u16x4*)(Av + ((size_t)db*TD_ + i)*3072 + 2048 + col) = z4v;
+        } else {
+          if (tid == 0) d_poll(bars, iM, 64);
+          __syncthreads();
+          const unsigned short* hq = hreg + p*16384 + db*H2_ + l*16;
+          u16x8 h0v = *(const u16x8*)hq;
+          u16x8 h1v = *(const u16x8*)(hq + 8);
+          float qf[16];
           #pragma unroll
-          for (int c = 0; c < 8; ++c) sc += qf[c]*bf2f(e0[c]);
+          for (int c = 0; c < 8; ++c){ qf[c] = bf2f(h0v[c]); qf[8+c] = bf2f(h1v[c]); }
+          for (int tp = wv; tp < i; tp += 4){
+            const unsigned short* vr = vbuf + ((size_t)tp*16 + db)*H2_ + l*16;
+            u16x8 e0 = *(const u16x8*)vr;
+            u16x8 e1 = *(const u16x8*)(vr + 8);
+            float sc = 0.f;
+            #pragma unroll
+            for (int c = 0; c < 8; ++c) sc += qf[c]*bf2f(e0[c]);
+            #pragma unroll
+            for (int c = 0; c < 8; ++c) sc += qf[8+c]*bf2f(e1[c]);
+            #pragma unroll
+            for (int o = 1; o < 64; o <<= 1) sc += __shfl_xor(sc, o);
+            if (l == 0) dscL[tp] = sc;
+          }
+          __syncthreads();
+          float scv = (l < i) ? dscL[l] : -1e30f;
+          float m = scv;
           #pragma unroll
-          for (int c = 0; c < 8; ++c) sc += qf[8+c]*bf2f(e1[c]);
+          for (int o = 1; o < 64; o <<= 1) m = fmaxf(m, __shfl_xor(m, o));
+          float e = (l < i) ? expf(scv - m) : 0.f;
+          float ssum = e;
           #pragma unroll
-          for (int o = 1; o < 64; o <<= 1) sc += __shfl_xor(sc, o);
-          if (l == 0) dscL[tp] = sc;
+          for (int o = 1; o < 64; o <<= 1) ssum += __shfl_xor(ssum, o);
+          float wgt = e / ssum;
+          float c0_=0.f,c1_=0.f,c2_=0.f,c3_=0.f;
+          for (int tp = 0; tp < i; ++tp){
+            float wt = __shfl(wgt, tp);
+            u16x4 hv = *(const u16x4*)(bufh + ((size_t)tp*16 + db)*H2_ + col);
+            c0_ += wt*bf2f(hv[0]); c1_ += wt*bf2f(hv[1]); c2_ += wt*bf2f(hv[2]); c3_ += wt*bf2f(hv[3]);
+          }
+          u16x4 o4; o4[0]=f2bf(c0_); o4[1]=f2bf(c1_); o4[2]=f2bf(c2_); o4[3]=f2bf(c3_);
+          *(u16x4*)(xbuf + (size_t)db*1024 + col) = o4;
+          *(u16x4*)(Av + ((size_t)db*TD_ + i)*3072 + 2048 + col) = o4;
         }
         __syncthreads();
-        float scv = (l < i) ? dscL[l] : -1e30f;
-        float m = scv;
-        #pragma unroll
-        for (int o = 1; o < 64; o <<= 1) m = fmaxf(m, __shfl_xor(m, o));
-        float e = (l < i) ? expf(scv - m) : 0.f;
-        float ssum = e;
-        #pragma unroll
-        for (int o = 1; o < 64; o <<= 1) ssum += __shfl_xor(ssum, o);
-        float wgt = e / ssum;
-        float c0_=0.f,c1_=0.f,c2_=0.f,c3_=0.f;
-        for (int tp = 0; tp < i; ++tp){
-          float wt = __shfl(wgt, tp);
-          u16x4 hv = *(const u16x4*)(bufh + ((size_t)tp*16 + db)*H2_ + col);
-          c0_ += wt*bf2f(hv[0]); c1_ += wt*bf2f(hv[1]); c2_ += wt*bf2f(hv[2]); c3_ += wt*bf2f(hv[3]);
-        }
-        u16x4 o4; o4[0]=f2bf(c0_); o4[1]=f2bf(c1_); o4[2]=f2bf(c2_); o4[3]=f2bf(c3_);
-        *(u16x4*)(xbuf + (size_t)db*1024 + col) = o4;
-        *(u16x4*)(Av + ((size_t)db*TD_ + i)*3072 + 2048 + col) = o4;
-      }
-      __syncthreads();
-      if (tid == 0){ arrive8(barA); poll8(barB, 64); __threadfence(); }
+      }
+      if (tid == 0) d_arrive(bars, iAb);
+      if (tid == 0) d_poll(bars, iBb, 64);
       __syncthreads();
     }
   }
@@ -875,14 +907,17 @@
   char* ws = (char*)d_ws;
 
   size_t o_bars   = 0;
-  size_t o_ctxn   = 327680;
+  size_t o_ctxn   = 397312;
   size_t o_psumT  = o_ctxn + 131072;
-  size_t o_xs     = o_psumT + 256;
+  size_t o_pz     = o_psumT + 256;
+  size_t o_xs     = o_pz + 262144;
   size_t o_decemb = o_xs + (size_t)6400*256*2;
   size_t o_Wenc   = o_decemb + (size_t)1024*256*2;
-  size_t o_WhExt  = o_Wenc + (size_t)2*2048*768*2;
-  size_t o_CtxW   = o_WhExt + (size_t)64*163840;
-  size_t o_Wemb   = o_CtxW + (size_t)64*262144;
+  size_t o_SA     = o_Wenc + (size_t)2*2048*768*2;
+  size_t o_SB     = o_SA + (size_t)64*98304;
+  size_t o_CA     = o_SB + (size_t)64*65536;
+  size_t o_CB     = o_CA + (size_t)64*131072;
+  size_t o_Wemb   = o_CB + (size_t)64*131072;
   size_t o_zinit  = o_Wemb + (size_t)4096*256*2;
   size_t o_zx     = o_zinit + (size_t)1024*4096*4;
   size_t o_enc    = o_zx + (size_t)2*6400*2048*2;
@@ -899,11 +934,14 @@
   unsigned* bars        = (unsigned*)(ws + o_bars);
   float* ctxn           = (float*)(ws + o_ctxn);
   float* psumT          = (float*)(ws + o_psumT);
+  float* pz             = (float*)(ws + o_pz);
   unsigned short* xs    = (unsigned short*)(ws + o_xs);
   unsigned short* decemb= (unsigned short*)(ws + o_decemb);
   unsigned short* Wenc  = (unsigned short*)(ws + o_Wenc);
-  char* WhExt           = ws + o_WhExt;
-  char* CtxW            = ws + o_CtxW;
+  char* SA              = ws + o_SA;
+  char* SB              = ws + o_SB;
+  char* CA              = ws + o_CA;
+  char* CB              = ws + o_CB;
   unsigned short* Wemb  = (unsigned short*)(ws + o_Wemb);
   float* zinit          = (float*)(ws + o_zinit);
   unsigned short* zx    = (unsigned short*)(ws + o_zx);
@@ -919,9 +957,9 @@
   unsigned short* Av    = (unsigned short*)(ws + o_Av);
 
   hipFuncSetAttribute((const void*)k_encoder, hipFuncAttributeMaxDynamicSharedMemorySize, 90000);
-  hipFuncSetAttribute((const void*)k_decoder, hipFuncAttributeMaxDynamicSharedMemorySize, 160768);
-
-  k_init<<<320, 256, 0, stream>>>(bars, ctxn, psumT);
+  hipFuncSetAttribute((const void*)k_decoder, hipFuncAttributeMaxDynamicSharedMemorySize, 107520);
+
+  k_init<<<392, 256, 0, stream>>>(bars, ctxn, psumT);
   k_gather<<<1600, 256, 0, stream>>>(emb, enc_in, xs, TE_);
   k_gather<<<256, 256, 0, stream>>>(emb, dec_in, decemb, TD_);
   k_prep_enc<<<1536, 256, 0, stream>>>(Wih_f, Whh_f, Wih_b, Whh_b, Wenc);
@@ -929,12 +967,12 @@
   k_zinit<<<256, 256, 0, stream>>>(decemb, Wemb, b_d, zinit);
   k_zx<<<1600, 256, 0, stream>>>(xs, Wenc, b_f, b_b, zx);
   k_encoder<<<208, 256, 87296, stream>>>(zx, Wenc, h0, c0, encO, hbuf, h0dec, c0dec, bars,
-                                         Whh_d, W_da, Wih_d, WhExt, CtxW);
+                                         Whh_d, W_da, Wih_d, SA, SB, CA, CB);
   k_penc<<<400, 256, 0, stream>>>(encO, W_ea, Penc);
   k_dec_init<<<64, 256, 0, stream>>>(h0dec, hreg);
-  k_decoder<<<208, 256, 160768, stream>>>(WhExt, CtxW, zinit, Penc, encO, c0dec,
+  k_decoder<<<256, 256, 107520, stream>>>(SA, SB, CA, CB, zinit, Penc, encO, c0dec,
                                           hreg, xbuf, ctxn, psumT, vbuf, bufh, Av,
-                                          out + (size_t)32768000, bars);
+                                          out + (size_t)32768000, pz, bars);
   k_vocab_gemm<<<2048, 256, 0, stream>>>(Av, W_v, b_v, out);
   k_logsoftmax<<<1024, 256, 0, stream>>>(out);
 }
```

Measured after the change: 6.217 ms. 1.12x slower.
